# Optimization experiments

Hardware: AMD Instinct MI355X
Metric: run time of the kernel (lower is better)

The kernel has to match this reference:

```python
import jax, jax.numpy as jnp
import numpy as np

N = 8388608          # number of samples (2**23)
T_MAX = 100000       # number of distinct time values -> ~84 ties per time


def setup_inputs() -> dict:
    key = jax.random.key(0)
    k1, k2, k3 = jax.random.split(key, 3)
    inp = jax.random.normal(k1, (N,), dtype=jnp.float32)            # log hazards
    target = jax.random.randint(k2, (N,), 0, T_MAX, dtype=jnp.int32)  # times
    weight = jax.random.randint(k3, (N,), 0, 2, dtype=jnp.int32)      # event indicator
    return {"input": inp, "target": target, "weight": weight}


def _cox_efron_npll(log_hz, time, event):
    """Negative Cox partial log-likelihood with Efron tie correction, mean reduction.

    Faithful to torchsurv's _partial_likelihood_efron: per unique time j,
    pll_j = sum_{i in H_j} log_hz_i - sum_{l=0}^{m_j-1} log(D_j - (l/m_j)*T_j)
    where H_j = events at time j, D_j = sum of exp(log_hz) over risk set (t>=t_j),
    T_j = sum of exp(log_hz) over H_j, m_j = |H_j|; loss = -mean over j with m_j>0.
    """
    n = log_hz.shape[0]
    order = jnp.argsort(time)                       # sort by time (group-sum math is tie-order invariant)
    t = time[order]
    lh = log_hz[order]
    ev = event[order].astype(lh.dtype)

    # group id per sample: 0..(num_unique-1), padded groups beyond that are empty
    new_grp = jnp.concatenate([jnp.zeros((1,), jnp.int32), (t[1:] != t[:-1]).astype(jnp.int32)])
    seg = jnp.cumsum(new_grp)                       # [n] int32

    hz = jnp.exp(lh)
    grp_hz = jax.ops.segment_sum(hz, seg, num_segments=n)          # sum exp per time group
    denom_naive = jnp.cumsum(grp_hz[::-1])[::-1]                   # risk-set sums (suffix over groups)
    m = jax.ops.segment_sum(ev, seg, num_segments=n)               # events per group
    log_nom = jax.ops.segment_sum(lh * ev, seg, num_segments=n)    # sum of log_hz over H_j
    ties = jax.ops.segment_sum(hz * ev, seg, num_segments=n)       # sum of exp over H_j

    # rank l in [0, m_j) of each event within its group
    csum_e = jnp.cumsum(ev)
    events_before = jnp.concatenate([jnp.zeros((1,), lh.dtype), jnp.cumsum(m)[:-1]])
    rank = csum_e - 1.0 - events_before[seg]
    mg = jnp.maximum(m[seg], 1.0)
    term = jnp.where(ev > 0.0,
                     jnp.log(denom_naive[seg] - (rank / mg) * ties[seg]),
                     0.0)
    log_denom = jax.ops.segment_sum(term, seg, num_segments=n)

    include = (m > 0.0).astype(lh.dtype)
    pll = jnp.where(m > 0.0, log_nom - log_denom, 0.0)
    # reduction='mean': -pll.nanmean() over groups that contain events
    return -(jnp.sum(pll) / jnp.sum(include))


def reference(input, target, weight):
    return _cox_efron_npll(input, target, weight)
```

## Files before the change

kernel.cpp:

```cpp
#include <hip/hip_runtime.h>

#define TMAXV 100000
#define CHUNK 256
#define NCHUNK ((TMAXV + CHUNK - 1) / CHUNK)
#define WB 256
#define LOGWB 8
#define SB ((TMAXV + WB - 1) / WB)
#define SBP 512
#define TILE 4096
#define RPT 16
#define KS 8
#define CAP 4096
#define RPH (CAP / 256)


__device__ __forceinline__ float block_reduce_sum(float v, float* sdata) {
    int lane = threadIdx.x & 63;
    int wid  = threadIdx.x >> 6;
    #pragma unroll
    for (int off = 32; off > 0; off >>= 1)
        v += __shfl_down(v, off, 64);
    if (lane == 0) sdata[wid] = v;
    __syncthreads();
    if (wid == 0) {
        v = (lane < 4) ? sdata[lane] : 0.0f;
        v += __shfl_down(v, 2, 64);
        v += __shfl_down(v, 1, 64);
    }
    return v;
}

__device__ __forceinline__ double block_reduce_sum_d(double v, double* sdata) {
    int lane = threadIdx.x & 63;
    int wid  = threadIdx.x >> 6;
    #pragma unroll
    for (int off = 32; off > 0; off >>= 1)
        v += __shfl_down(v, off, 64);
    if (lane == 0) sdata[wid] = v;
    __syncthreads();
    if (wid == 0) {
        v = (lane < 4) ? sdata[lane] : 0.0;
        v += __shfl_down(v, 2, 64);
        v += __shfl_down(v, 1, 64);
    }
    return v;
}

__device__ __forceinline__ unsigned encode_rec(float x, int t, int e) {
    float h = __expf(x);
    return (__float_as_uint(h) & 0x7FFFFF00u)
         | (unsigned)(t & (WB - 1))
         | ((unsigned)e << 31);
}


__global__ void count_pfx_kernel(const int* __restrict__ tgt,
                                 int* __restrict__ pfx_arr,
                                 int* __restrict__ cnt_t, int n) {
    __shared__ int lc[SBP];
    __shared__ int ls[SBP];
    int tid = threadIdx.x, tile = blockIdx.x;
    lc[tid] = 0; lc[tid + 256] = 0;
    __syncthreads();
    int lo = tile * TILE;
    if (lo + TILE <= n) {
        const int4* tgt4 = (const int4*)(tgt + lo);
        #pragma unroll
        for (int q = 0; q < RPT / 4; ++q) {
            int4 t4 = tgt4[q * 256 + tid];
            atomicAdd(&lc[t4.x >> LOGWB], 1);
            atomicAdd(&lc[t4.y >> LOGWB], 1);
            atomicAdd(&lc[t4.z >> LOGWB], 1);
            atomicAdd(&lc[t4.w >> LOGWB], 1);
        }
    } else {
        int hi = min(n, lo + TILE);
        for (int i = lo + tid; i < hi; i += 256)
            atomicAdd(&lc[tgt[i] >> LOGWB], 1);
    }
    __syncthreads();
    int c0 = lc[tid], c1 = lc[tid + 256];
    int i1 = tid + 256;
    ls[tid] = c0; ls[i1] = c1;
    __syncthreads();
    for (int off = 1; off < SBP; off <<= 1) {
        int a0 = (tid >= off) ? ls[tid - off] : 0;
        int a1 = (i1  >= off) ? ls[i1  - off] : 0;
        __syncthreads();
        ls[tid] += a0; ls[i1] += a1;
        __syncthreads();
    }
    size_t rb = (size_t)tile * SBP;
    pfx_arr[rb + tid] = ls[tid] - c0;
    pfx_arr[rb + i1]  = ls[i1]  - c1;
    cnt_t[rb + tid] = c0;
    cnt_t[rb + i1]  = c1;
}

__global__ void tile_scan_direct_kernel(const int* __restrict__ cnt_t,
                                        int* __restrict__ tilebase_s,
                                        int* __restrict__ totals, int nt) {
    __shared__ int ls[256];
    int s = blockIdx.x, tid = threadIdx.x;
    int run = 0;
    for (int t0 = 0; t0 < nt; t0 += 256) {
        int t = t0 + tid;
        int c = (t < nt) ? cnt_t[(size_t)t * SBP + s] : 0;
        ls[tid] = c;
        __syncthreads();
        for (int off = 1; off < 256; off <<= 1) {
            int a = (tid >= off) ? ls[tid - off] : 0;
            __syncthreads();
            ls[tid] += a;
            __syncthreads();
        }
        int incl = ls[tid];
        int tot  = ls[255];
        if (t < nt) tilebase_s[(size_t)s * nt + t] = run + incl - c;
        run += tot;
        __syncthreads();
    }
    if (tid == 0) totals[s] = run;
}

__global__ void bucket_base_kernel(const int* __restrict__ totals,
                                   int* __restrict__ base, int n) {
    __shared__ int ls[SBP];
    int tid = threadIdx.x;
    int c = totals[tid];
    ls[tid] = c;
    __syncthreads();
    for (int off = 1; off < SBP; off <<= 1) {
        int a = (tid >= off) ? ls[tid - off] : 0;
        __syncthreads();
        ls[tid] += a;
        __syncthreads();
    }
    base[tid] = ls[tid] - c;
    if (tid == 0) base[SBP] = n;
}

__global__ void scatter_kernel(const float* __restrict__ lh,
                               const int*   __restrict__ tgt,
                               const int*   __restrict__ ev,
                               const int*   __restrict__ pfx_arr,
                               const int*   __restrict__ tilebase_s,
                               const int*   __restrict__ base,
                               unsigned* __restrict__ val,
                               double* __restrict__ acc, int n, int nt) {
    __shared__ unsigned fu[TILE];
    __shared__ unsigned short bidv[TILE];
    __shared__ int pfx[SBP];
    __shared__ int tb[SBP];
    __shared__ int lrank[SBP];
    __shared__ float sdata[4];
    int tid  = threadIdx.x;
    int tile = blockIdx.x;
    int lo   = tile * TILE;
    int cnt_here = min(TILE, n - lo);
    int i1 = tid + 256;
    size_t rb = (size_t)tile * SBP;

    pfx[tid] = pfx_arr[rb + tid];
    pfx[i1]  = pfx_arr[rb + i1];
    tb[tid]  = base[tid] + tilebase_s[(size_t)tid * nt + tile];
    tb[i1]   = base[i1]  + tilebase_s[(size_t)i1  * nt + tile];
    lrank[tid] = 0; lrank[i1] = 0;

    unsigned rbits[RPT];
    int      rk[RPT];
    float xl = 0.f;
    if (lo + TILE <= n) {
        const int4*   tgt4 = (const int4*)(tgt + lo);
        const int4*   ev4  = (const int4*)(ev + lo);
        const float4* lh4  = (const float4*)(lh + lo);
        #pragma unroll
        for (int q = 0; q < RPT / 4; ++q) {
            int idx = q * 256 + tid;
            int4   t4 = tgt4[idx];
            int4   e4 = ev4[idx];
            float4 x4 = lh4[idx];
            rbits[q*4+0] = encode_rec(x4.x, t4.x, e4.x & 1); rk[q*4+0] = t4.x >> LOGWB; if (e4.x & 1) xl += x4.x;
            rbits[q*4+1] = encode_rec(x4.y, t4.y, e4.y & 1); rk[q*4+1] = t4.y >> LOGWB; if (e4.y & 1) xl += x4.y;
            rbits[q*4+2] = encode_rec(x4.z, t4.z, e4.z & 1); rk[q*4+2] = t4.z >> LOGWB; if (e4.z & 1) xl += x4.z;
            rbits[q*4+3] = encode_rec(x4.w, t4.w, e4.w & 1); rk[q*4+3] = t4.w >> LOGWB; if (e4.w & 1) xl += x4.w;
        }
    } else {
        #pragma unroll
        for (int k = 0; k < RPT; ++k) {
            int i = lo + k * 256 + tid;
            if (i < n) {
                int t = tgt[i]; int e = ev[i] & 1; float x = lh[i];
                rbits[k] = encode_rec(x, t, e);
                rk[k] = t >> LOGWB;
                if (e) xl += x;
            } else rk[k] = -1;
        }
    }
    __syncthreads();

    #pragma unroll
    for (int k = 0; k < RPT; ++k) {
        if (rk[k] >= 0) {
            int b = rk[k];
            int r = atomicAdd(&lrank[b], 1);
            int pos = pfx[b] + r;
            fu[pos]   = rbits[k];
            bidv[pos] = (unsigned short)b;
        }
    }
    __syncthreads();

    int pairs = cnt_here >> 1;
    const uint2* fu2 = (const uint2*)fu;
    const unsigned* bid2 = (const unsigned*)bidv;
    for (int q = tid; q < pairs; q += 256) {
        uint2 bb = fu2[q];
        unsigned bp = bid2[q];
        int b0 = (int)(bp & 0xFFFFu);
        int b1 = (int)(bp >> 16);
        int p0 = q * 2;
        val[tb[b0] + (p0     - pfx[b0])] = bb.x;
        val[tb[b1] + (p0 + 1 - pfx[b1])] = bb.y;
    }
    if ((cnt_here & 1) && tid == 0) {
        int p = cnt_here - 1;
        int b = (int)bidv[p];
        val[tb[b] + (p - pfx[b])] = fu[p];
    }

    float rl = block_reduce_sum(xl, sdata);
    if (tid == 0) atomicAdd(&acc[2], (double)rl);
}

__global__ void bucket_hist_kernel(const unsigned* __restrict__ val,
                                   const int* __restrict__ base,
                                   float* __restrict__ partials,
                                   float* __restrict__ chunk_sum) {
    __shared__ unsigned fv[CAP];
    __shared__ unsigned cnt[WB];
    __shared__ unsigned rankc[WB];
    __shared__ unsigned pfx[WB];
    __shared__ unsigned ls[WB];
    __shared__ float sdata[4];
    int tid = threadIdx.x;
    int b   = blockIdx.x >> 3;
    int k   = blockIdx.x & (KS - 1);
    int lo0 = base[b], len = base[b + 1] - lo0;
    int lo  = lo0 + (int)(((long long)len * k) / KS);
    int hi  = lo0 + (int)(((long long)len * (k + 1)) / KS);

    float sh = 0.f, cm = 0.f, th = 0.f;

    for (int c0 = lo; c0 < hi; c0 += CAP) {
        int c1 = min(hi, c0 + CAP);
        cnt[tid] = 0; rankc[tid] = 0;
        __syncthreads();

        unsigned rv[RPH];
        int      rs[RPH];
        #pragma unroll
        for (int u = 0; u < RPH; ++u) {
            int i = c0 + u * 256 + tid;
            if (i < c1) {
                rv[u] = val[i];
                rs[u] = (int)(rv[u] & (WB - 1));
                atomicAdd(&cnt[rs[u]], 1u);
            } else {
                rs[u] = -1;
            }
        }
        __syncthreads();

        unsigned c = cnt[tid];
        ls[tid] = c;
        __syncthreads();
        for (int off = 1; off < 256; off <<= 1) {
            unsigned a = (tid >= off) ? ls[tid - off] : 0u;
            __syncthreads();
            ls[tid] += a;
            __syncthreads();
        }
        pfx[tid] = ls[tid] - c;
        __syncthreads();

        #pragma unroll
        for (int u = 0; u < RPH; ++u) {
            if (rs[u] >= 0) {
                unsigned r = atomicAdd(&rankc[rs[u]], 1u);
                fv[pfx[rs[u]] + r] = rv[u];
            }
        }
        __syncthreads();

        int s0 = (int)pfx[tid], e0 = s0 + (int)cnt[tid];
        for (int p = s0; p < e0; ++p) {
            unsigned bits = fv[p];
            float h = fabsf(__uint_as_float(bits));
            sh += h;
            if (bits >> 31) { cm += 1.0f; th += h; }
        }
        __syncthreads();
    }

    float* pbase = partials + (size_t)blockIdx.x * 3 * WB;
    pbase[0 * WB + tid] = sh;
    pbase[1 * WB + tid] = cm;
    pbase[2 * WB + tid] = th;

    float st = block_reduce_sum(sh, sdata);
    if (tid == 0) unsafeAtomicAdd(&chunk_sum[b], st);
}

__global__ void pll_suffix_kernel(const float* __restrict__ partials,
                                  const float* __restrict__ chunk_sum,
                                  double* __restrict__ acc) {
    __shared__ float sf[CHUNK];
    __shared__ float sdata[4];
    __shared__ float sdata2[4];
    __shared__ double dsd[4];
    __shared__ double doff;
    int tid = threadIdx.x;
    int b   = blockIdx.x;
    float sh = 0.f, cm = 0.f, th = 0.f;
    #pragma unroll
    for (int k = 0; k < KS; ++k) {
        const float* pbase = partials + (size_t)(b * KS + k) * 3 * WB;
        sh += pbase[0 * WB + tid];
        cm += pbase[1 * WB + tid];
        th += pbase[2 * WB + tid];
    }
    sf[tid] = sh;
    __syncthreads();
    for (int off = 1; off < CHUNK; off <<= 1) {
        float add = (tid + off < CHUNK) ? sf[tid + off] : 0.0f;
        __syncthreads();
        sf[tid] += add;
        __syncthreads();
    }
    double mysum = 0.0;
    for (int j = b + 1 + tid; j < NCHUNK; j += 256)
        mysum += (double)chunk_sum[j];
    double red = block_reduce_sum_d(mysum, dsd);
    if (tid == 0) doff = red;
    __syncthreads();
    double off_d = doff;

    int t = b * CHUNK + tid;
    float pll = 0.0f, inc = 0.0f;
    if (t < TMAXV && cm > 0.5f) {
        float D    = (float)(off_d + (double)sf[tid]);
        int   mi   = (int)(cm + 0.5f);
        float step = th / cm;
        float s = 0.0f;
        for (int l = 0; l < mi; ++l)
            s += __logf(D - (float)l * step);
        pll = -s;
        inc = 1.0f;
    }
    float rp = block_reduce_sum(pll, sdata);
    __syncthreads();
    float ri = block_reduce_sum(inc, sdata2);
    if (threadIdx.x == 0) {
        atomicAdd(&acc[0], (double)rp);
        atomicAdd(&acc[1], (double)ri);
    }
}

__global__ void finalize_kernel(const double* __restrict__ acc,
                                float* __restrict__ out) {
    double cnt = acc[1];
    out[0] = (cnt > 0.0) ? (float)(-(acc[0] + acc[2]) / cnt) : 0.0f;
}

__global__ void hist_kernel(const float* __restrict__ lh,
                            const int*   __restrict__ tgt,
                            const int*   __restrict__ ev,
                            float* __restrict__ sum_hz,
                            float* __restrict__ mcnt,
                            float* __restrict__ log_nom,
                            float* __restrict__ ties,
                            int n) {
    int i = blockIdx.x * blockDim.x + threadIdx.x;
    if (i >= n) return;
    float x = lh[i];
    int   t = tgt[i];
    int   e = ev[i];
    float h = __expf(x);
    unsafeAtomicAdd(&sum_hz[t], h);
    if (e) {
        unsafeAtomicAdd(&mcnt[t], 1.0f);
        unsafeAtomicAdd(&log_nom[t], x);
        unsafeAtomicAdd(&ties[t], h);
    }
}

__global__ void chunk_sum_kernel(const float* __restrict__ sum_hz,
                                 float* __restrict__ chunk_sum) {
    __shared__ float sdata[4];
    int i = blockIdx.x * CHUNK + threadIdx.x;
    float v = (i < TMAXV) ? sum_hz[i] : 0.0f;
    v = block_reduce_sum(v, sdata);
    if (threadIdx.x == 0) chunk_sum[blockIdx.x] = v;
}

__global__ void chunk_scan_kernel(const float* __restrict__ chunk_sum,
                                  double* __restrict__ chunk_off) {
    __shared__ double ds[512];
    int tid = threadIdx.x;
    double own = (tid < NCHUNK) ? (double)chunk_sum[tid] : 0.0;
    ds[tid] = own;
    __syncthreads();
    for (int off = 1; off < 512; off <<= 1) {
        double add = (tid + off < 512) ? ds[tid + off] : 0.0;
        __syncthreads();
        ds[tid] += add;
        __syncthreads();
    }
    if (tid < NCHUNK) chunk_off[tid] = ds[tid] - own;
}

__global__ void pll_kernel(const float* __restrict__ mcnt,
                           const float* __restrict__ log_nom,
                           const float* __restrict__ ties,
                           const float* __restrict__ sum_hz,
                           const double* __restrict__ chunk_off,
                           double* __restrict__ acc) {
    __shared__ float sf[CHUNK];
    __shared__ float sdata[4];
    __shared__ float sdata2[4];
    int tid = threadIdx.x;
    int t   = blockIdx.x * CHUNK + tid;
    float v = (t < TMAXV) ? sum_hz[t] : 0.0f;
    sf[tid] = v;
    __syncthreads();
    for (int off = 1; off < CHUNK; off <<= 1) {
        float add = (tid + off < CHUNK) ? sf[tid + off] : 0.0f;
        __syncthreads();
        sf[tid] += add;
        __syncthreads();
    }
    float pll = 0.0f, inc = 0.0f;
    if (t < TMAXV) {
        float mv = mcnt[t];
        if (mv > 0.5f) {
            float D    = (float)(chunk_off[blockIdx.x] + (double)sf[tid]);
            float T    = ties[t];
            int   mi   = (int)(mv + 0.5f);
            float step = T / mv;
            float s = 0.0f;
            for (int l = 0; l < mi; ++l)
                s += __logf(D - (float)l * step);
            pll = log_nom[t] - s;
            inc = 1.0f;
        }
    }
    float rp = block_reduce_sum(pll, sdata);
    __syncthreads();
    float ri = block_reduce_sum(inc, sdata2);
    if (threadIdx.x == 0) {
        atomicAdd(&acc[0], (double)rp);
        atomicAdd(&acc[1], (double)ri);
    }
}

extern "C" void kernel_launch(void* const* d_in, const int* in_sizes, int n_in,
                              void* d_out, int out_size, void* d_ws, size_t ws_size,
                              hipStream_t stream) {
    const float* lh  = (const float*)d_in[0];
    const int*   tgt = (const int*)d_in[1];
    const int*   ev  = (const int*)d_in[2];
    float*       out = (float*)d_out;
    int n  = in_sizes[0];
    int nt = (n + TILE - 1) / TILE;

    char* ws = (char*)d_ws;
    size_t off = 0;
    auto take = [&](size_t bytes, size_t align) {
        off = (off + align - 1) & ~(align - 1);
        size_t r = off; off += bytes; return r;
    };
    size_t o_acc    = take(32, 16);
    size_t o_csum   = take((size_t)SBP * 4, 16);
    size_t zero_bytes = off;
    size_t o_base   = take((size_t)(SBP + 1) * 4, 16);
    size_t o_totals = take((size_t)SBP * 4, 16);
    size_t o_pfx    = take((size_t)nt * SBP * 4, 16);
    size_t o_cntt   = take((size_t)nt * SBP * 4, 16);
    size_t o_tbs    = take((size_t)nt * SBP * 4, 16);
    size_t o_val    = take((size_t)n * 4, 16);
    size_t need     = off;
    size_t part_sz  = (size_t)SB * KS * 3 * WB * 4;
    size_t o_part   = o_pfx;
    if (o_part + part_sz > need) need = o_part + part_sz;

    if (ws_size >= need) {
        double*   acc       = (double*)(ws + o_acc);
        float*    chunk_sum = (float*)(ws + o_csum);
        int*      base      = (int*)(ws + o_base);
        int*      totals    = (int*)(ws + o_totals);
        int*      pfx_arr   = (int*)(ws + o_pfx);
        int*      cnt_t     = (int*)(ws + o_cntt);
        int*      tilebase_s= (int*)(ws + o_tbs);
        unsigned* val       = (unsigned*)(ws + o_val);
        float*    partials  = (float*)(ws + o_part);

        hipMemsetAsync(d_ws, 0, zero_bytes, stream);

        count_pfx_kernel<<<nt, 256, 0, stream>>>(tgt, pfx_arr, cnt_t, n);
        tile_scan_direct_kernel<<<SBP, 256, 0, stream>>>(cnt_t, tilebase_s, totals, nt);
        bucket_base_kernel<<<1, SBP, 0, stream>>>(totals, base, n);
        scatter_kernel<<<nt, 256, 0, stream>>>(lh, tgt, ev, pfx_arr, tilebase_s, base,
                                               val, acc, n, nt);
        bucket_hist_kernel<<<SB * KS, 256, 0, stream>>>(val, base, partials, chunk_sum);
        pll_suffix_kernel<<<NCHUNK, 256, 0, stream>>>(partials, chunk_sum, acc);
        finalize_kernel<<<1, 1, 0, stream>>>(acc, out);
    } else {
        size_t f = 0;
        auto ftake = [&](size_t bytes, size_t align) {
            f = (f + align - 1) & ~(align - 1);
            size_t r = f; f += bytes; return r;
        };
        size_t f_acc  = ftake(32, 16);
        size_t f_sum  = ftake((size_t)TMAXV * 4, 16);
        size_t f_m    = ftake((size_t)TMAXV * 4, 16);
        size_t f_ln   = ftake((size_t)TMAXV * 4, 16);
        size_t f_ties = ftake((size_t)TMAXV * 4, 16);
        size_t zb     = f;
        size_t f_csum = ftake((size_t)NCHUNK * 4, 16);
        size_t f_coff = ftake((size_t)NCHUNK * 8, 8);

        double* acc     = (double*)(ws + f_acc);
        float*  sum_hz  = (float*)(ws + f_sum);
        float*  mcnt    = (float*)(ws + f_m);
        float*  log_nom = (float*)(ws + f_ln);
        float*  ties    = (float*)(ws + f_ties);
        float*  chunk_sum = (float*)(ws + f_csum);
        double* chunk_off = (double*)(ws + f_coff);

        hipMemsetAsync(d_ws, 0, zb, stream);

        hist_kernel<<<(n + 255) / 256, 256, 0, stream>>>(lh, tgt, ev, sum_hz, mcnt, log_nom, ties, n);
        chunk_sum_kernel<<<NCHUNK, 256, 0, stream>>>(sum_hz, chunk_sum);
        chunk_scan_kernel<<<1, 512, 0, stream>>>(chunk_sum, chunk_off);
        pll_kernel<<<NCHUNK, 256, 0, stream>>>(mcnt, log_nom, ties, sum_hz, chunk_off, acc);
        finalize_kernel<<<1, 1, 0, stream>>>(acc, out);
    }
}
```

Before: 217.9 us.

## Widen time buckets to 512 so scatter uses byte bucket ids and 4-wide writes

Doubles the per-bucket time width from 256 to 512, halving the number of coarse buckets (SB about 196, padded to 256). The count/prefix and scatter kernels drop to one bucket slot per thread, and bucket ids fit in a byte, so the scatter writeback moves to quads. The histogram kernel now runs 512 threads per block with KS=16 splits and emits two chunk sums per bucket, which the suffix kernel maps back with a half index. The intent is to cut scan and sync overhead in the sort-like passes, at the cost of one fewer mantissa bit in the packed hazard and a larger partials buffer that no longer aliases the prefix arrays.

```diff
diff --git a/kernel.cpp b/kernel.cpp
--- a/kernel.cpp
+++ b/kernel.cpp
@@ -3,15 +3,15 @@
 #define TMAXV 100000
 #define CHUNK 256
 #define NCHUNK ((TMAXV + CHUNK - 1) / CHUNK)
-#define WB 256
-#define LOGWB 8
+#define WB 512
+#define LOGWB 9
 #define SB ((TMAXV + WB - 1) / WB)
-#define SBP 512
+#define SBW 256
 #define TILE 4096
 #define RPT 16
-#define KS 8
+#define KS 16
 #define CAP 4096
-#define RPH (CAP / 256)
+#define RPH (CAP / 512)
 
 
 __device__ __forceinline__ float block_reduce_sum(float v, float* sdata) {
@@ -48,7 +48,7 @@
 
 __device__ __forceinline__ unsigned encode_rec(float x, int t, int e) {
     float h = __expf(x);
-    return (__float_as_uint(h) & 0x7FFFFF00u)
+    return (__float_as_uint(h) & 0x7FFFFE00u)
          | (unsigned)(t & (WB - 1))
          | ((unsigned)e << 31);
 }
@@ -57,10 +57,10 @@
 __global__ void count_pfx_kernel(const int* __restrict__ tgt,
                                  int* __restrict__ pfx_arr,
                                  int* __restrict__ cnt_t, int n) {
-    __shared__ int lc[SBP];
-    __shared__ int ls[SBP];
+    __shared__ int lc[SBW];
+    __shared__ int ls[SBW];
     int tid = threadIdx.x, tile = blockIdx.x;
-    lc[tid] = 0; lc[tid + 256] = 0;
+    lc[tid] = 0;
     __syncthreads();
     int lo = tile * TILE;
     if (lo + TILE <= n) {
@@ -79,22 +79,18 @@
             atomicAdd(&lc[tgt[i] >> LOGWB], 1);
     }
     __syncthreads();
-    int c0 = lc[tid], c1 = lc[tid + 256];
-    int i1 = tid + 256;
-    ls[tid] = c0; ls[i1] = c1;
-    __syncthreads();
-    for (int off = 1; off < SBP; off <<= 1) {
-        int a0 = (tid >= off) ? ls[tid - off] : 0;
-        int a1 = (i1  >= off) ? ls[i1  - off] : 0;
-        __syncthreads();
-        ls[tid] += a0; ls[i1] += a1;
-        __syncthreads();
-    }
-    size_t rb = (size_t)tile * SBP;
-    pfx_arr[rb + tid] = ls[tid] - c0;
-    pfx_arr[rb + i1]  = ls[i1]  - c1;
-    cnt_t[rb + tid] = c0;
-    cnt_t[rb + i1]  = c1;
+    int c = lc[tid];
+    ls[tid] = c;
+    __syncthreads();
+    for (int off = 1; off < SBW; off <<= 1) {
+        int a = (tid >= off) ? ls[tid - off] : 0;
+        __syncthreads();
+        ls[tid] += a;
+        __syncthreads();
+    }
+    size_t rb = (size_t)tile * SBW;
+    pfx_arr[rb + tid] = ls[tid] - c;
+    cnt_t[rb + tid]   = c;
 }
 
 __global__ void tile_scan_direct_kernel(const int* __restrict__ cnt_t,
@@ -105,7 +101,7 @@
     int run = 0;
     for (int t0 = 0; t0 < nt; t0 += 256) {
         int t = t0 + tid;
-        int c = (t < nt) ? cnt_t[(size_t)t * SBP + s] : 0;
+        int c = (t < nt) ? cnt_t[(size_t)t * SBW + s] : 0;
         ls[tid] = c;
         __syncthreads();
         for (int off = 1; off < 256; off <<= 1) {
@@ -125,19 +121,19 @@
 
 __global__ void bucket_base_kernel(const int* __restrict__ totals,
                                    int* __restrict__ base, int n) {
-    __shared__ int ls[SBP];
+    __shared__ int ls[SBW];
     int tid = threadIdx.x;
     int c = totals[tid];
     ls[tid] = c;
     __syncthreads();
-    for (int off = 1; off < SBP; off <<= 1) {
+    for (int off = 1; off < SBW; off <<= 1) {
         int a = (tid >= off) ? ls[tid - off] : 0;
         __syncthreads();
         ls[tid] += a;
         __syncthreads();
     }
     base[tid] = ls[tid] - c;
-    if (tid == 0) base[SBP] = n;
+    if (tid == 0) base[SBW] = n;
 }
 
 __global__ void scatter_kernel(const float* __restrict__ lh,
@@ -149,23 +145,20 @@
                                unsigned* __restrict__ val,
                                double* __restrict__ acc, int n, int nt) {
     __shared__ unsigned fu[TILE];
-    __shared__ unsigned short bidv[TILE];
-    __shared__ int pfx[SBP];
-    __shared__ int tb[SBP];
-    __shared__ int lrank[SBP];
+    __shared__ unsigned char bidv[TILE];
+    __shared__ int pfx[SBW];
+    __shared__ int tb[SBW];
+    __shared__ int lrank[SBW];
     __shared__ float sdata[4];
     int tid  = threadIdx.x;
     int tile = blockIdx.x;
     int lo   = tile * TILE;
     int cnt_here = min(TILE, n - lo);
-    int i1 = tid + 256;
-    size_t rb = (size_t)tile * SBP;
+    size_t rb = (size_t)tile * SBW;
 
     pfx[tid] = pfx_arr[rb + tid];
-    pfx[i1]  = pfx_arr[rb + i1];
     tb[tid]  = base[tid] + tilebase_s[(size_t)tid * nt + tile];
-    tb[i1]   = base[i1]  + tilebase_s[(size_t)i1  * nt + tile];
-    lrank[tid] = 0; lrank[i1] = 0;
+    lrank[tid] = 0;
 
     unsigned rbits[RPT];
     int      rk[RPT];
@@ -206,25 +199,26 @@
             int r = atomicAdd(&lrank[b], 1);
             int pos = pfx[b] + r;
             fu[pos]   = rbits[k];
-            bidv[pos] = (unsigned short)b;
-        }
-    }
-    __syncthreads();
-
-    int pairs = cnt_here >> 1;
-    const uint2* fu2 = (const uint2*)fu;
-    const unsigned* bid2 = (const unsigned*)bidv;
-    for (int q = tid; q < pairs; q += 256) {
-        uint2 bb = fu2[q];
-        unsigned bp = bid2[q];
-        int b0 = (int)(bp & 0xFFFFu);
-        int b1 = (int)(bp >> 16);
-        int p0 = q * 2;
+            bidv[pos] = (unsigned char)b;
+        }
+    }
+    __syncthreads();
+
+    int quads = cnt_here >> 2;
+    const uint4* fu4 = (const uint4*)fu;
+    const unsigned* bid4 = (const unsigned*)bidv;
+    for (int q = tid; q < quads; q += 256) {
+        uint4 bb = fu4[q];
+        unsigned bp = bid4[q];
+        int p0 = q * 4;
+        int b0 = (int)(bp & 255u), b1 = (int)((bp >> 8) & 255u);
+        int b2 = (int)((bp >> 16) & 255u), b3 = (int)(bp >> 24);
         val[tb[b0] + (p0     - pfx[b0])] = bb.x;
         val[tb[b1] + (p0 + 1 - pfx[b1])] = bb.y;
-    }
-    if ((cnt_here & 1) && tid == 0) {
-        int p = cnt_here - 1;
+        val[tb[b2] + (p0 + 2 - pfx[b2])] = bb.z;
+        val[tb[b3] + (p0 + 3 - pfx[b3])] = bb.w;
+    }
+    for (int p = quads * 4 + tid; p < cnt_here; p += 256) {
         int b = (int)bidv[p];
         val[tb[b] + (p - pfx[b])] = fu[p];
     }
@@ -242,9 +236,9 @@
     __shared__ unsigned rankc[WB];
     __shared__ unsigned pfx[WB];
     __shared__ unsigned ls[WB];
-    __shared__ float sdata[4];
+    __shared__ float swv[8];
     int tid = threadIdx.x;
-    int b   = blockIdx.x >> 3;
+    int b   = blockIdx.x >> 4;
     int k   = blockIdx.x & (KS - 1);
     int lo0 = base[b], len = base[b + 1] - lo0;
     int lo  = lo0 + (int)(((long long)len * k) / KS);
@@ -261,7 +255,7 @@
         int      rs[RPH];
         #pragma unroll
         for (int u = 0; u < RPH; ++u) {
-            int i = c0 + u * 256 + tid;
+            int i = c0 + u * 512 + tid;
             if (i < c1) {
                 rv[u] = val[i];
                 rs[u] = (int)(rv[u] & (WB - 1));
@@ -275,7 +269,7 @@
         unsigned c = cnt[tid];
         ls[tid] = c;
         __syncthreads();
-        for (int off = 1; off < 256; off <<= 1) {
+        for (int off = 1; off < WB; off <<= 1) {
             unsigned a = (tid >= off) ? ls[tid - off] : 0u;
             __syncthreads();
             ls[tid] += a;
@@ -308,8 +302,23 @@
     pbase[1 * WB + tid] = cm;
     pbase[2 * WB + tid] = th;
 
-    float st = block_reduce_sum(sh, sdata);
-    if (tid == 0) unsafeAtomicAdd(&chunk_sum[b], st);
+    {
+        int lane = tid & 63, wid = tid >> 6;
+        float v = sh;
+        #pragma unroll
+        for (int off = 32; off > 0; off >>= 1)
+            v += __shfl_down(v, off, 64);
+        if (lane == 0) swv[wid] = v;
+        __syncthreads();
+        if (tid == 0) {
+            float s = swv[0] + swv[1] + swv[2] + swv[3];
+            unsafeAtomicAdd(&chunk_sum[2 * b], s);
+        }
+        if (tid == 1) {
+            float s = swv[4] + swv[5] + swv[6] + swv[7];
+            unsafeAtomicAdd(&chunk_sum[2 * b + 1], s);
+        }
+    }
 }
 
 __global__ void pll_suffix_kernel(const float* __restrict__ partials,
@@ -322,10 +331,12 @@
     __shared__ double doff;
     int tid = threadIdx.x;
     int b   = blockIdx.x;
+    int B   = b >> 1;
+    int h   = b & 1;
     float sh = 0.f, cm = 0.f, th = 0.f;
-    #pragma unroll
+    #pragma unroll 4
     for (int k = 0; k < KS; ++k) {
-        const float* pbase = partials + (size_t)(b * KS + k) * 3 * WB;
+        const float* pbase = partials + (size_t)(B * KS + k) * 3 * WB + h * 256;
         sh += pbase[0 * WB + tid];
         cm += pbase[1 * WB + tid];
         th += pbase[2 * WB + tid];
@@ -481,18 +492,16 @@
         size_t r = off; off += bytes; return r;
     };
     size_t o_acc    = take(32, 16);
-    size_t o_csum   = take((size_t)SBP * 4, 16);
+    size_t o_csum   = take((size_t)(2 * SB + 2) * 4, 16);
     size_t zero_bytes = off;
-    size_t o_base   = take((size_t)(SBP + 1) * 4, 16);
-    size_t o_totals = take((size_t)SBP * 4, 16);
-    size_t o_pfx    = take((size_t)nt * SBP * 4, 16);
-    size_t o_cntt   = take((size_t)nt * SBP * 4, 16);
-    size_t o_tbs    = take((size_t)nt * SBP * 4, 16);
+    size_t o_base   = take((size_t)(SBW + 1) * 4, 16);
+    size_t o_totals = take((size_t)SBW * 4, 16);
+    size_t o_pfx    = take((size_t)nt * SBW * 4, 16);
+    size_t o_cntt   = take((size_t)nt * SBW * 4, 16);
+    size_t o_tbs    = take((size_t)SBW * nt * 4, 16);
     size_t o_val    = take((size_t)n * 4, 16);
+    size_t o_part   = take((size_t)SB * KS * 3 * WB * 4, 16);
     size_t need     = off;
-    size_t part_sz  = (size_t)SB * KS * 3 * WB * 4;
-    size_t o_part   = o_pfx;
-    if (o_part + part_sz > need) need = o_part + part_sz;
 
     if (ws_size >= need) {
         double*   acc       = (double*)(ws + o_acc);
@@ -508,11 +517,11 @@
         hipMemsetAsync(d_ws, 0, zero_bytes, stream);
 
         count_pfx_kernel<<<nt, 256, 0, stream>>>(tgt, pfx_arr, cnt_t, n);
-        tile_scan_direct_kernel<<<SBP, 256, 0, stream>>>(cnt_t, tilebase_s, totals, nt);
-        bucket_base_kernel<<<1, SBP, 0, stream>>>(totals, base, n);
+        tile_scan_direct_kernel<<<SBW, 256, 0, stream>>>(cnt_t, tilebase_s, totals, nt);
+        bucket_base_kernel<<<1, SBW, 0, stream>>>(totals, base, n);
         scatter_kernel<<<nt, 256, 0, stream>>>(lh, tgt, ev, pfx_arr, tilebase_s, base,
                                                val, acc, n, nt);
-        bucket_hist_kernel<<<SB * KS, 256, 0, stream>>>(val, base, partials, chunk_sum);
+        bucket_hist_kernel<<<SB * KS, 512, 0, stream>>>(val, base, partials, chunk_sum);
         pll_suffix_kernel<<<NCHUNK, 256, 0, stream>>>(partials, chunk_sum, acc);
         finalize_kernel<<<1, 1, 0, stream>>>(acc, out);
     } else {
```

New measurement: 218.5 us. No clear change (+0.3%).
